# Kernel optimization log

Measured on AMD Instinct MI355X. Metric: run time of the kernel, lower is better.

Reference implementation:

```python
import jax, jax.numpy as jnp
import numpy as np

N_NODES = 50000
N_EDGES = 800000
D_IN = 96
D_OUT = 96


def setup_inputs() -> dict:
    key = jax.random.key(0)
    k1, k2, k3, k4 = jax.random.split(key, 4)
    feat = jax.random.normal(k1, (N_NODES, D_IN), dtype=jnp.float32)
    # xavier_normal-like init for weight, zeros bias (as in the torch module)
    std = (2.0 / (D_IN + D_OUT)) ** 0.5
    weight = jax.random.normal(k2, (D_IN, D_OUT), dtype=jnp.float32) * std
    bias = jnp.zeros((D_OUT,), dtype=jnp.float32)
    src = jax.random.randint(k3, (N_EDGES,), 0, N_NODES, dtype=jnp.int64)
    dst = jax.random.randint(k4, (N_EDGES,), 0, N_NODES, dtype=jnp.int64)
    return {"feat": feat, "weight": weight, "bias": bias, "src": src, "dst": dst}


def reference(feat, weight, bias, src, dst):
    N = feat.shape[0]
    ones = jnp.ones(src.shape[0], dtype=feat.dtype)
    out_deg = jax.ops.segment_sum(ones, src, num_segments=N)  # out-degree per node
    in_deg = jax.ops.segment_sum(ones, dst, num_segments=N)   # in-degree per node
    ci = jnp.clip(out_deg, 1.0, None) ** -0.5                 # src-side norm
    cj = jnp.clip(in_deg, 1.0, None) ** -0.5                  # dst-side norm
    # gather src features * ci, scatter-sum to dst, scale by cj
    msg = feat[src] * ci[src, None]                           # [E, D_IN]
    agg = jax.ops.segment_sum(msg, dst, num_segments=N) * cj[:, None]
    # DGL UDF reduce only updates nodes that receive messages; isolated
    # (zero in-degree) nodes keep their original features.
    h = jnp.where(in_deg[:, None] > 0, agg, feat)
    return jnp.matmul(h, weight) + bias
```

## Files before the change

kernel.cpp:

```cpp
#include <hip/hip_runtime.h>

#define N_NODES 50000
#define N_EDGES 800000
#define D 96
#define D4 (D / 4)

#define RL 12
#define HPAD 13
#define CONV_BLOCKS ((N_NODES * RL + 255) / 256)
#define WPREP_BLOCKS ((D * (D / 2) + 255) / 256)

#define NB 196
#define ECAP 5120
#define CCAP 6144
#define PA_BLOCKS 200
#define PA_CHUNK 4000

typedef __attribute__((ext_vector_type(8))) short short8;
typedef __attribute__((ext_vector_type(4))) float floatx4;

__device__ __forceinline__ short8 as_short8(uint4 u) { return *(short8*)&u; }

__device__ __forceinline__ unsigned bf16pack(float a, float b) {
    unsigned ua = __float_as_uint(a);
    unsigned ub = __float_as_uint(b);
    ua = (ua + 0x7FFFu + ((ua >> 16) & 1u)) >> 16;
    ub = (ub + 0x7FFFu + ((ub >> 16) & 1u)) & 0xFFFF0000u;
    return ua | ub;
}

__global__ void __launch_bounds__(1024) sortA_kernel(
        const int* __restrict__ src, const int* __restrict__ dst,
        int* __restrict__ deg_out, unsigned* __restrict__ gcur,
        unsigned* __restrict__ ebuf) {
    __shared__ unsigned raw[PA_CHUNK];
    __shared__ unsigned ord[PA_CHUNK];
    __shared__ unsigned hist[NB], lstart[NB], cur[NB], gbase[NB];
    __shared__ unsigned sc[256];
    int t = threadIdx.x;
    int e0 = blockIdx.x * PA_CHUNK;
    for (int i = t; i < NB; i += 1024) hist[i] = 0;
    __syncthreads();
    for (int i = t; i < PA_CHUNK; i += 1024) {
        int s = src[e0 + i];
        int d = dst[e0 + i];
        raw[i] = ((unsigned)d << 16) | (unsigned)s;
        atomicAdd(&deg_out[s], 1);
        atomicAdd(&hist[d >> 8], 1);
    }
    __syncthreads();
    if (t < 256) sc[t] = (t < NB) ? hist[t] : 0;
    __syncthreads();
    for (int o = 1; o < 256; o <<= 1) {
        unsigned v = 0;
        if (t < 256 && t >= o) v = sc[t - o];
        __syncthreads();
        if (t < 256 && t >= o) sc[t] += v;
        __syncthreads();
    }
    if (t < NB) {
        unsigned ls = sc[t] - hist[t];
        lstart[t] = ls;
        cur[t] = ls;
        gbase[t] = atomicAdd(&gcur[t], hist[t]);
    }
    __syncthreads();
    for (int i = t; i < PA_CHUNK; i += 1024) {
        unsigned r = raw[i];
        unsigned b = r >> 24;
        unsigned p = atomicAdd(&cur[b], 1);
        ord[p] = r;
    }
    __syncthreads();
    for (int i = t; i < PA_CHUNK; i += 1024) {
        unsigned r = ord[i];
        unsigned b = r >> 24;
        unsigned pos = gbase[b] + ((unsigned)i - lstart[b]);
        if (pos < ECAP) ebuf[b * ECAP + pos] = r;
    }
}

__global__ void __launch_bounds__(1024) sortB_kernel(
        const unsigned* __restrict__ gcur, const unsigned* __restrict__ ebuf,
        int* __restrict__ deg_in, int* __restrict__ off,
        unsigned short* __restrict__ csr) {
    __shared__ unsigned eb[ECAP];
    __shared__ unsigned short csr_l[CCAP];
    __shared__ unsigned dcount[256], dcur[256], sc[256];
    int b = blockIdx.x;
    int t = threadIdx.x;
    unsigned cnt = gcur[b];
    if (cnt > ECAP) cnt = ECAP;
    for (int i = t; i < 256; i += 1024) dcount[i] = 0;
    __syncthreads();
    const unsigned* __restrict__ sg = ebuf + (size_t)b * ECAP;
    for (int i = t; i < (int)cnt; i += 1024) {
        unsigned r = sg[i];
        eb[i] = r;
        atomicAdd(&dcount[(r >> 16) & 255u], 1);
    }
    __syncthreads();
    if (t < 256) sc[t] = (dcount[t] + 7u) & ~7u;
    __syncthreads();
    for (int o = 1; o < 256; o <<= 1) {
        unsigned v = 0;
        if (t < 256 && t >= o) v = sc[t - o];
        __syncthreads();
        if (t < 256 && t >= o) sc[t] += v;
        __syncthreads();
    }
    if (t < 256) {
        int n = b * 256 + t;
        unsigned ex = sc[t] - ((dcount[t] + 7u) & ~7u);
        dcur[t] = ex;
        if (n < N_NODES) {
            deg_in[n] = (int)dcount[t];
            off[n] = b * CCAP + (int)ex;
        }
    }
    __syncthreads();
    for (int i = t; i < (int)cnt; i += 1024) {
        unsigned r = eb[i];
        unsigned p = atomicAdd(&dcur[(r >> 16) & 255u], 1);
        if (p < CCAP) csr_l[p] = (unsigned short)(r & 0xFFFFu);
    }
    __syncthreads();
    unsigned tot = sc[255];
    if (tot > CCAP) tot = CCAP;
    unsigned* __restrict__ og = (unsigned*)(csr + (size_t)b * CCAP);
    const unsigned* __restrict__ cl = (const unsigned*)csr_l;
    for (int i = t; i < (int)(tot >> 1); i += 1024) og[i] = cl[i];
}

__global__ void __launch_bounds__(256) conv_kernel(
        const float4* __restrict__ feat4, const int* __restrict__ deg_out,
        uint4* __restrict__ sfeat, const float* __restrict__ W,
        unsigned* __restrict__ WT32) {
    int blk = blockIdx.x;
    if (blk >= CONV_BLOCKS) {
        int t = (blk - CONV_BLOCKS) * 256 + threadIdx.x;
        if (t >= D * (D / 2)) return;
        int n = t / (D / 2);
        int j = t - n * (D / 2);
        float w0 = W[(2 * j) * D + n];
        float w1 = W[(2 * j + 1) * D + n];
        WT32[n * (D / 2) + j] = bf16pack(w0, w1);
        return;
    }
    int t = blk * 256 + threadIdx.x;
    if (t >= N_NODES * RL) return;
    int n = t / RL;
    int lane = t - n * RL;
    float c = rsqrtf(fmaxf((float)deg_out[n], 1.0f));
    float4 a = feat4[n * D4 + lane * 2];
    float4 b = feat4[n * D4 + lane * 2 + 1];
    uint4 o;
    o.x = bf16pack(a.x * c, a.y * c);
    o.y = bf16pack(a.z * c, a.w * c);
    o.z = bf16pack(b.x * c, b.y * c);
    o.w = bf16pack(b.z * c, b.w * c);
    sfeat[t] = o;
}

__global__ void __launch_bounds__(192) gather_mm_kernel(
        const float4* __restrict__ feat4, const uint4* __restrict__ sfeat,
        const int* __restrict__ deg_in, const int* __restrict__ off,
        const unsigned short* __restrict__ csr, const uint4* __restrict__ wt4,
        const float* __restrict__ bias, float* __restrict__ out) {
    __shared__ uint4 sh[16 * HPAD];
    int tid = threadIdx.x;
    {
        int g = tid / RL;
        int lane = tid - g * RL;
        int n = blockIdx.x * 16 + g;
        int deg = deg_in[n];
        uint4* __restrict__ hout = &sh[g * HPAD + lane];
        if (deg == 0) {
            float4 a = feat4[n * D4 + lane * 2];
            float4 b = feat4[n * D4 + lane * 2 + 1];
            uint4 o;
            o.x = bf16pack(a.x, a.y);
            o.y = bf16pack(a.z, a.w);
            o.z = bf16pack(b.x, b.y);
            o.w = bf16pack(b.z, b.w);
            *hout = o;
        } else {
            const unsigned short* __restrict__ bk = csr + off[n];
            const uint4* __restrict__ sf = sfeat + lane;
            float acc[8] = {};
#define ACC8(v)  { \
        acc[0] += __uint_as_float((v).x << 16); \
        acc[1] += __uint_as_float((v).x & 0xFFFF0000u); \
        acc[2] += __uint_as_float((v).y << 16); \
        acc[3] += __uint_as_float((v).y & 0xFFFF0000u); \
        acc[4] += __uint_as_float((v).z << 16); \
        acc[5] += __uint_as_float((v).z & 0xFFFF0000u); \
        acc[6] += __uint_as_float((v).w << 16); \
        acc[7] += __uint_as_float((v).w & 0xFFFF0000u); }
            int full = deg & ~7;
            int i = 0;
            for (; i < full; i += 8) {
                uint4 idx = *(const uint4*)(bk + i);
                unsigned s0 = idx.x & 0xFFFFu, s1 = idx.x >> 16;
                unsigned s2 = idx.y & 0xFFFFu, s3 = idx.y >> 16;
                unsigned s4 = idx.z & 0xFFFFu, s5 = idx.z >> 16;
                unsigned s6 = idx.w & 0xFFFFu, s7 = idx.w >> 16;
                uint4 v0 = sf[(size_t)s0 * RL];
                uint4 v1 = sf[(size_t)s1 * RL];
                uint4 v2 = sf[(size_t)s2 * RL];
                uint4 v3 = sf[(size_t)s3 * RL];
                uint4 v4 = sf[(size_t)s4 * RL];
                uint4 v5 = sf[(size_t)s5 * RL];
                uint4 v6 = sf[(size_t)s6 * RL];
                uint4 v7 = sf[(size_t)s7 * RL];
                ACC8(v0); ACC8(v1); ACC8(v2); ACC8(v3);
                ACC8(v4); ACC8(v5); ACC8(v6); ACC8(v7);
            }
            for (; i < deg; ++i) {
                uint4 v = sf[(size_t)bk[i] * RL];
                ACC8(v);
            }
#undef ACC8
            float cj = rsqrtf((float)deg);
            uint4 o;
            o.x = bf16pack(acc[0] * cj, acc[1] * cj);
            o.y = bf16pack(acc[2] * cj, acc[3] * cj);
            o.z = bf16pack(acc[4] * cj, acc[5] * cj);
            o.w = bf16pack(acc[6] * cj, acc[7] * cj);
            *hout = o;
        }
    }
    __syncthreads();
    int wave = tid >> 6;
    int lane = tid & 63;
    int m = lane & 15, quad = lane >> 4;
    short8 a0 = as_short8(sh[m * HPAD + quad]);
    short8 a1 = as_short8(sh[m * HPAD + 4 + quad]);
    short8 a2 = as_short8(sh[m * HPAD + 8 + quad]);
    int row0 = blockIdx.x * 16;
    int r_out0 = row0 + quad * 4;
#pragma unroll
    for (int ct = wave * 2; ct < wave * 2 + 2; ++ct) {
        int n = ct * 16 + m;
        int wb = n * RL + quad;
        short8 b0 = as_short8(wt4[wb]);
        short8 b1 = as_short8(wt4[wb + 4]);
        short8 b2 = as_short8(wt4[wb + 8]);
        floatx4 c = {0.f, 0.f, 0.f, 0.f};
        c = __builtin_amdgcn_mfma_f32_16x16x32_bf16(a0, b0, c, 0, 0, 0);
        c = __builtin_amdgcn_mfma_f32_16x16x32_bf16(a1, b1, c, 0, 0, 0);
        c = __builtin_amdgcn_mfma_f32_16x16x32_bf16(a2, b2, c, 0, 0, 0);
        float bs = bias[n];
#pragma unroll
        for (int r = 0; r < 4; ++r)
            out[(size_t)(r_out0 + r) * D + n] = c[r] + bs;
    }
}

extern "C" void kernel_launch(void* const* d_in, const int* in_sizes, int n_in,
                              void* d_out, int out_size, void* d_ws, size_t ws_size,
                              hipStream_t stream) {
    const float* feat = (const float*)d_in[0];
    const float* W    = (const float*)d_in[1];
    const float* bias = (const float*)d_in[2];
    const int*   src  = (const int*)d_in[3];
    const int*   dst  = (const int*)d_in[4];

    int*            deg_out = (int*)d_ws;
    unsigned*       gcur    = (unsigned*)(deg_out + N_NODES);
    int*            deg_in  = (int*)(gcur + NB);
    int*            off     = deg_in + N_NODES;
    unsigned*       ebuf    = (unsigned*)(off + N_NODES);
    unsigned short* csr     = (unsigned short*)(ebuf + (size_t)NB * ECAP);
    uint4*          sfeat   = (uint4*)((char*)csr + (size_t)NB * CCAP * 2);
    unsigned*       WT32    = (unsigned*)(sfeat + (size_t)N_NODES * RL);

    hipMemsetAsync(deg_out, 0, (N_NODES + NB) * sizeof(int), stream);
    sortA_kernel<<<PA_BLOCKS, 1024, 0, stream>>>(src, dst, deg_out, gcur, ebuf);
    sortB_kernel<<<NB, 1024, 0, stream>>>(gcur, ebuf, deg_in, off, csr);
    conv_kernel<<<CONV_BLOCKS + WPREP_BLOCKS, 256, 0, stream>>>(
        (const float4*)feat, deg_out, sfeat, W, WT32);
    gather_mm_kernel<<<N_NODES / 16, 192, 0, stream>>>(
        (const float4*)feat, sfeat, deg_in, off, csr, (const uint4*)WT32,
        bias, (float*)d_out);
}
```

Measured before the change: 159.7 us.

## Bucket-sort src ids to compute out-degree without global atomics; unroll gather by 16

Out-degree counting moves from per-edge global atomics into the two-pass bucket sort. sortA now also bins source ids into per-bucket short buffers, and sortB counts them in shared memory and writes deg_out directly, so only the small gcur counters need a memset. sortA runs with more blocks and smaller chunks, and the gather loop gains a 16-wide unrolled stage to keep more loads in flight. The cost is extra shared-memory traffic and a second scatter in sortA, higher register pressure in the gather, and silent truncation if a source bucket overflows SCAP.

Result: faster. 138.8 us (-13.1%).

```diff
diff --git a/kernel.cpp b/kernel.cpp
--- a/kernel.cpp
+++ b/kernel.cpp
@@ -12,9 +12,10 @@
 
 #define NB 196
 #define ECAP 5120
+#define SCAP 5120
 #define CCAP 6144
-#define PA_BLOCKS 200
-#define PA_CHUNK 4000
+#define PA_BLOCKS 256
+#define PA_CHUNK 3125
 
 typedef __attribute__((ext_vector_type(8))) short short8;
 typedef __attribute__((ext_vector_type(4))) float floatx4;
@@ -31,25 +32,88 @@
 
 __global__ void __launch_bounds__(1024) sortA_kernel(
         const int* __restrict__ src, const int* __restrict__ dst,
-        int* __restrict__ deg_out, unsigned* __restrict__ gcur,
-        unsigned* __restrict__ ebuf) {
+        unsigned* __restrict__ gcur,
+        unsigned* __restrict__ ebuf, unsigned short* __restrict__ sbuf) {
     __shared__ unsigned raw[PA_CHUNK];
     __shared__ unsigned ord[PA_CHUNK];
-    __shared__ unsigned hist[NB], lstart[NB], cur[NB], gbase[NB];
-    __shared__ unsigned sc[256];
+    __shared__ unsigned short sord[PA_CHUNK];
+    __shared__ unsigned hist[512];
+    __shared__ unsigned sc[512], lstart[512], cur[512], gbase[512];
     int t = threadIdx.x;
     int e0 = blockIdx.x * PA_CHUNK;
-    for (int i = t; i < NB; i += 1024) hist[i] = 0;
+    if (t < 512) hist[t] = 0;
     __syncthreads();
     for (int i = t; i < PA_CHUNK; i += 1024) {
         int s = src[e0 + i];
         int d = dst[e0 + i];
         raw[i] = ((unsigned)d << 16) | (unsigned)s;
-        atomicAdd(&deg_out[s], 1);
-        atomicAdd(&hist[d >> 8], 1);
-    }
-    __syncthreads();
-    if (t < 256) sc[t] = (t < NB) ? hist[t] : 0;
+        atomicAdd(&hist[d >> 8], 1u);
+        atomicAdd(&hist[256 + (s >> 8)], 1u);
+    }
+    __syncthreads();
+    if (t < 512) sc[t] = hist[t];
+    __syncthreads();
+    for (int o = 1; o < 256; o <<= 1) {
+        unsigned v = 0;
+        if (t < 512 && (t & 255) >= o) v = sc[t - o];
+        __syncthreads();
+        if (t < 512 && (t & 255) >= o) sc[t] += v;
+        __syncthreads();
+    }
+    if (t < 512) {
+        unsigned ls = sc[t] - hist[t];
+        lstart[t] = ls;
+        cur[t] = ls;
+        if ((t & 255) < NB)
+            gbase[t] = atomicAdd(&gcur[(t >> 8) * NB + (t & 255)], hist[t]);
+    }
+    __syncthreads();
+    for (int i = t; i < PA_CHUNK; i += 1024) {
+        unsigned r = raw[i];
+        unsigned p = atomicAdd(&cur[r >> 24], 1u);
+        ord[p] = r;
+        unsigned s = r & 0xFFFFu;
+        unsigned q = atomicAdd(&cur[256 + (s >> 8)], 1u);
+        sord[q] = (unsigned short)s;
+    }
+    __syncthreads();
+    for (int i = t; i < PA_CHUNK; i += 1024) {
+        unsigned r = ord[i];
+        unsigned bd = r >> 24;
+        unsigned pos = gbase[bd] + ((unsigned)i - lstart[bd]);
+        if (pos < ECAP) ebuf[bd * ECAP + pos] = r;
+        unsigned s = sord[i];
+        unsigned bs = 256 + (s >> 8);
+        unsigned pos2 = gbase[bs] + ((unsigned)i - lstart[bs]);
+        if (pos2 < SCAP) sbuf[(size_t)(bs - 256) * SCAP + pos2] = (unsigned short)s;
+    }
+}
+
+__global__ void __launch_bounds__(1024) sortB_kernel(
+        const unsigned* __restrict__ gcur, const unsigned* __restrict__ ebuf,
+        const unsigned short* __restrict__ sbuf,
+        int* __restrict__ deg_out, int* __restrict__ deg_in,
+        int* __restrict__ off, unsigned short* __restrict__ csr) {
+    __shared__ unsigned eb[ECAP];
+    __shared__ unsigned short csr_l[CCAP];
+    __shared__ unsigned dcount[256], dcur[256], scount[256], sc[256];
+    int b = blockIdx.x;
+    int t = threadIdx.x;
+    unsigned cntd = gcur[b];      if (cntd > ECAP) cntd = ECAP;
+    unsigned cnts = gcur[NB + b]; if (cnts > SCAP) cnts = SCAP;
+    if (t < 256) { dcount[t] = 0; scount[t] = 0; }
+    __syncthreads();
+    const unsigned* __restrict__ sg = ebuf + (size_t)b * ECAP;
+    for (int i = t; i < (int)cntd; i += 1024) {
+        unsigned r = sg[i];
+        eb[i] = r;
+        atomicAdd(&dcount[(r >> 16) & 255u], 1u);
+    }
+    const unsigned short* __restrict__ ss = sbuf + (size_t)b * SCAP;
+    for (int i = t; i < (int)cnts; i += 1024)
+        atomicAdd(&scount[ss[i] & 255u], 1u);
+    __syncthreads();
+    if (t < 256) sc[t] = (dcount[t] + 7u) & ~7u;
     __syncthreads();
     for (int o = 1; o < 256; o <<= 1) {
         unsigned v = 0;
@@ -58,70 +122,20 @@
         if (t < 256 && t >= o) sc[t] += v;
         __syncthreads();
     }
-    if (t < NB) {
-        unsigned ls = sc[t] - hist[t];
-        lstart[t] = ls;
-        cur[t] = ls;
-        gbase[t] = atomicAdd(&gcur[t], hist[t]);
-    }
-    __syncthreads();
-    for (int i = t; i < PA_CHUNK; i += 1024) {
-        unsigned r = raw[i];
-        unsigned b = r >> 24;
-        unsigned p = atomicAdd(&cur[b], 1);
-        ord[p] = r;
-    }
-    __syncthreads();
-    for (int i = t; i < PA_CHUNK; i += 1024) {
-        unsigned r = ord[i];
-        unsigned b = r >> 24;
-        unsigned pos = gbase[b] + ((unsigned)i - lstart[b]);
-        if (pos < ECAP) ebuf[b * ECAP + pos] = r;
-    }
-}
-
-__global__ void __launch_bounds__(1024) sortB_kernel(
-        const unsigned* __restrict__ gcur, const unsigned* __restrict__ ebuf,
-        int* __restrict__ deg_in, int* __restrict__ off,
-        unsigned short* __restrict__ csr) {
-    __shared__ unsigned eb[ECAP];
-    __shared__ unsigned short csr_l[CCAP];
-    __shared__ unsigned dcount[256], dcur[256], sc[256];
-    int b = blockIdx.x;
-    int t = threadIdx.x;
-    unsigned cnt = gcur[b];
-    if (cnt > ECAP) cnt = ECAP;
-    for (int i = t; i < 256; i += 1024) dcount[i] = 0;
-    __syncthreads();
-    const unsigned* __restrict__ sg = ebuf + (size_t)b * ECAP;
-    for (int i = t; i < (int)cnt; i += 1024) {
-        unsigned r = sg[i];
-        eb[i] = r;
-        atomicAdd(&dcount[(r >> 16) & 255u], 1);
-    }
-    __syncthreads();
-    if (t < 256) sc[t] = (dcount[t] + 7u) & ~7u;
-    __syncthreads();
-    for (int o = 1; o < 256; o <<= 1) {
-        unsigned v = 0;
-        if (t < 256 && t >= o) v = sc[t - o];
-        __syncthreads();
-        if (t < 256 && t >= o) sc[t] += v;
-        __syncthreads();
-    }
     if (t < 256) {
         int n = b * 256 + t;
         unsigned ex = sc[t] - ((dcount[t] + 7u) & ~7u);
         dcur[t] = ex;
         if (n < N_NODES) {
-            deg_in[n] = (int)dcount[t];
+            deg_in[n]  = (int)dcount[t];
+            deg_out[n] = (int)scount[t];
             off[n] = b * CCAP + (int)ex;
         }
     }
     __syncthreads();
-    for (int i = t; i < (int)cnt; i += 1024) {
+    for (int i = t; i < (int)cntd; i += 1024) {
         unsigned r = eb[i];
-        unsigned p = atomicAdd(&dcur[(r >> 16) & 255u], 1);
+        unsigned p = atomicAdd(&dcur[(r >> 16) & 255u], 1u);
         if (p < CCAP) csr_l[p] = (unsigned short)(r & 0xFFFFu);
     }
     __syncthreads();
@@ -197,9 +211,42 @@
         acc[5] += __uint_as_float((v).z & 0xFFFF0000u); \
         acc[6] += __uint_as_float((v).w << 16); \
         acc[7] += __uint_as_float((v).w & 0xFFFF0000u); }
-            int full = deg & ~7;
             int i = 0;
-            for (; i < full; i += 8) {
+            int full16 = deg & ~15;
+            for (; i < full16; i += 16) {
+                uint4 ia = *(const uint4*)(bk + i);
+                uint4 ib = *(const uint4*)(bk + i + 8);
+                unsigned s0 = ia.x & 0xFFFFu, s1 = ia.x >> 16;
+                unsigned s2 = ia.y & 0xFFFFu, s3 = ia.y >> 16;
+                unsigned s4 = ia.z & 0xFFFFu, s5 = ia.z >> 16;
+                unsigned s6 = ia.w & 0xFFFFu, s7 = ia.w >> 16;
+                unsigned s8 = ib.x & 0xFFFFu, s9 = ib.x >> 16;
+                unsigned sa = ib.y & 0xFFFFu, sb = ib.y >> 16;
+                unsigned sx = ib.z & 0xFFFFu, sd = ib.z >> 16;
+                unsigned se = ib.w & 0xFFFFu, sfi = ib.w >> 16;
+                uint4 v0 = sf[(size_t)s0 * RL];
+                uint4 v1 = sf[(size_t)s1 * RL];
+                uint4 v2 = sf[(size_t)s2 * RL];
+                uint4 v3 = sf[(size_t)s3 * RL];
+                uint4 v4 = sf[(size_t)s4 * RL];
+                uint4 v5 = sf[(size_t)s5 * RL];
+                uint4 v6 = sf[(size_t)s6 * RL];
+                uint4 v7 = sf[(size_t)s7 * RL];
+                uint4 v8 = sf[(size_t)s8 * RL];
+                uint4 v9 = sf[(size_t)s9 * RL];
+                uint4 va = sf[(size_t)sa * RL];
+                uint4 vb = sf[(size_t)sb * RL];
+                uint4 vc = sf[(size_t)sx * RL];
+                uint4 vd = sf[(size_t)sd * RL];
+                uint4 ve = sf[(size_t)se * RL];
+                uint4 vf = sf[(size_t)sfi * RL];
+                ACC8(v0); ACC8(v1); ACC8(v2); ACC8(v3);
+                ACC8(v4); ACC8(v5); ACC8(v6); ACC8(v7);
+                ACC8(v8); ACC8(v9); ACC8(va); ACC8(vb);
+                ACC8(vc); ACC8(vd); ACC8(ve); ACC8(vf);
+            }
+            int full8 = deg & ~7;
+            for (; i < full8; i += 8) {
                 uint4 idx = *(const uint4*)(bk + i);
                 unsigned s0 = idx.x & 0xFFFFu, s1 = idx.x >> 16;
                 unsigned s2 = idx.y & 0xFFFFu, s3 = idx.y >> 16;
@@ -266,18 +313,19 @@
     const int*   src  = (const int*)d_in[3];
     const int*   dst  = (const int*)d_in[4];
 
-    int*            deg_out = (int*)d_ws;
-    unsigned*       gcur    = (unsigned*)(deg_out + N_NODES);
-    int*            deg_in  = (int*)(gcur + NB);
+    unsigned*       gcur    = (unsigned*)d_ws;
+    int*            deg_out = (int*)(gcur + 2 * NB);
+    int*            deg_in  = deg_out + N_NODES;
     int*            off     = deg_in + N_NODES;
     unsigned*       ebuf    = (unsigned*)(off + N_NODES);
-    unsigned short* csr     = (unsigned short*)(ebuf + (size_t)NB * ECAP);
-    uint4*          sfeat   = (uint4*)((char*)csr + (size_t)NB * CCAP * 2);
+    unsigned short* sbuf    = (unsigned short*)(ebuf + (size_t)NB * ECAP);
+    unsigned short* csr     = sbuf + (size_t)NB * SCAP;
+    uint4*          sfeat   = (uint4*)(csr + (size_t)NB * CCAP);
     unsigned*       WT32    = (unsigned*)(sfeat + (size_t)N_NODES * RL);
 
-    hipMemsetAsync(deg_out, 0, (N_NODES + NB) * sizeof(int), stream);
-    sortA_kernel<<<PA_BLOCKS, 1024, 0, stream>>>(src, dst, deg_out, gcur, ebuf);
-    sortB_kernel<<<NB, 1024, 0, stream>>>(gcur, ebuf, deg_in, off, csr);
+    hipMemsetAsync(gcur, 0, 2 * NB * sizeof(unsigned), stream);
+    sortA_kernel<<<PA_BLOCKS, 1024, 0, stream>>>(src, dst, gcur, ebuf, sbuf);
+    sortB_kernel<<<NB, 1024, 0, stream>>>(gcur, ebuf, sbuf, deg_out, deg_in, off, csr);
     conv_kernel<<<CONV_BLOCKS + WPREP_BLOCKS, 256, 0, stream>>>(
         (const float4*)feat, deg_out, sfeat, W, WT32);
     gather_mm_kernel<<<N_NODES / 16, 192, 0, stream>>>(
```
